# Kernel tuning notes

Measured on AMD Instinct MI355X. Metric: run time of the kernel, lower is better.

## Reference

```python
import math
import jax, jax.numpy as jnp
import numpy as np

N_HEAD = 16
NUM_BUCKETS = 32
MAX_DISTANCE = 2048
NEG_INF = -1e9  # finite stand-in for -inf in masked_fill; rows always have >=1 unmasked entry


def _relative_position_bucket(relative_position, num_buckets=NUM_BUCKETS, max_distance=MAX_DISTANCE):
    # causal (bidirectional=False) T5 bucketing
    rp = -jnp.minimum(relative_position, 0)  # nonneg distances
    max_exact = num_buckets // 2
    is_small = rp < max_exact
    rp_safe = jnp.maximum(rp, 1).astype(jnp.float32)
    large = max_exact + (
        jnp.log(rp_safe / max_exact) / math.log(max_distance / max_exact) * (num_buckets - max_exact)
    ).astype(jnp.int32)
    large = jnp.minimum(large, num_buckets - 1)
    return jnp.where(is_small, rp, large)


def t5_bias(rel_table, T):
    ctx = jnp.arange(T)[:, None]
    mem = jnp.arange(T)[None, :]
    buckets = _relative_position_bucket(mem - ctx)        # [T, T]
    bias = rel_table[buckets]                              # [T, T, H]
    return jnp.transpose(bias, (2, 0, 1))                  # [H, T, T]


def setup_inputs() -> dict:
    key = jax.random.key(0)
    k1, k2, k3, k4 = jax.random.split(key, 4)
    B, T, C = 2, 2048, 1024
    x = jax.random.normal(k1, (B, T, C), dtype=jnp.float32)
    w_qkv = jax.random.normal(k2, (C, 3 * C), dtype=jnp.float32) * (1.0 / math.sqrt(C))
    w_proj = jax.random.normal(k3, (C, C), dtype=jnp.float32) * (1.0 / math.sqrt(C))
    rel_table = jax.random.normal(k4, (NUM_BUCKETS, N_HEAD), dtype=jnp.float32) * 0.02
    return {"x": x, "w_qkv": w_qkv, "w_proj": w_proj, "rel_table": rel_table}


def reference(x, w_qkv, w_proj, rel_table):
    B, T, C = x.shape
    H = N_HEAD
    d = C // H
    qkv = x @ w_qkv                                        # [B, T, 3C]
    q, k, v = jnp.split(qkv, 3, axis=-1)
    q = q.reshape(B, T, H, d).transpose(0, 2, 1, 3)        # [B, H, T, d]
    k = k.reshape(B, T, H, d).transpose(0, 2, 1, 3)
    v = v.reshape(B, T, H, d).transpose(0, 2, 1, 3)

    bias = t5_bias(rel_table, T)                           # [H, T, T]
    causal = jnp.tril(jnp.ones((T, T), dtype=bool))
    bias = jnp.where(causal[None], bias, NEG_INF)          # masked_fill(-inf) on bias

    scores = jnp.einsum("bhqd,bhkd->bhqk", q, k) * (1.0 / math.sqrt(d))
    scores = scores + bias[None]                           # broadcast over batch
    att = jax.nn.softmax(scores, axis=-1)
    y = jnp.einsum("bhqk,bhkd->bhqd", att, v)              # [B, H, T, d]
    y = y.transpose(0, 2, 1, 3).reshape(B, T, C)
    return y @ w_proj
```

## Files before the change

kernel.cpp:

```cpp
#include <hip/hip_runtime.h>
#include <hip/hip_bf16.h>
#include <cstdint>
#include <cstddef>

#define B_  2
#define T_  2048
#define C_  1024
#define H_  16
#define D_  64
#define NEG_INF_ -1e9f

typedef short bf16x8 __attribute__((ext_vector_type(8)));
typedef float f32x4  __attribute__((ext_vector_type(4)));

__device__ __forceinline__ short f2bf(float f) {
  union { float f; unsigned u; } x; x.f = f;
  unsigned r = (x.u + 0x7fffu + ((x.u >> 16) & 1u)) >> 16;
  return (short)r;
}

__device__ __forceinline__ void gload16(const void* g, void* l) {
  __builtin_amdgcn_global_load_lds(
      (const __attribute__((address_space(1))) unsigned int*)g,
      (__attribute__((address_space(3))) unsigned int*)l, 16, 0, 0);
}

__global__ __launch_bounds__(256) void cvt_bf16(const float* __restrict__ in,
                                                short* __restrict__ out, int n4) {
  int i = blockIdx.x * 256 + threadIdx.x;
  if (i < n4) {
    float4 v = ((const float4*)in)[i];
    short4 o;
    o.x = f2bf(v.x); o.y = f2bf(v.y); o.z = f2bf(v.z); o.w = f2bf(v.w);
    ((short4*)out)[i] = o;
  }
}

__global__ __launch_bounds__(256) void transpose_cvt(const float* __restrict__ in,
                                                     short* __restrict__ out,
                                                     int R, int C) {
  __shared__ float tile[32][33];
  int gx = blockIdx.x * 32, gy = blockIdx.y * 32;
  int tx = threadIdx.x, ty = threadIdx.y;
#pragma unroll
  for (int i = 0; i < 4; ++i)
    tile[ty + i * 8][tx] = in[(size_t)(gy + ty + i * 8) * C + gx + tx];
  __syncthreads();
#pragma unroll
  for (int i = 0; i < 4; ++i)
    out[(size_t)(gx + ty + i * 8) * R + gy + tx] = f2bf(tile[tx][ty + i * 8]);
}

__global__ __launch_bounds__(256) void bias_table(const float* __restrict__ rel_table,
                                                  float* __restrict__ btab) {
  int idx = blockIdx.x * 256 + threadIdx.x;
  if (idx >= H_ * T_) return;
  int dist = idx & (T_ - 1);
  int h = idx >> 11;
  int bucket;
  if (dist < 16) {
    bucket = dist;
  } else {
    float rp = (float)dist;
    int large = 16 + (int)(logf(rp * (1.0f / 16.0f)) * (1.0f / logf(128.0f)) * 16.0f);
    bucket = large < 31 ? large : 31;
  }
  btab[idx] = rel_table[bucket * H_ + h];
}

template <int MODE>
__global__ __launch_bounds__(256) void gemm_bt128(
    const short* __restrict__ A, const short* __restrict__ Bt,
    int M, int N, int K,
    short* __restrict__ q_out, short* __restrict__ k_out,
    short* __restrict__ vT_out, float* __restrict__ f_out) {
  __shared__ alignas(16) short As[128 * 64];
  __shared__ alignas(16) short Bs[128 * 64];
  const int tid = threadIdx.x;
  const int w = tid >> 6, lane = tid & 63;
  const int g = lane >> 4, l16 = lane & 15;
  const int wr = w >> 1, wc = w & 1;
  const int m0 = blockIdx.y * 128, n0 = blockIdx.x * 128;

  const char* Ag = (const char*)(A + (size_t)m0 * K);
  const char* Bg = (const char*)(Bt + (size_t)n0 * K);
  char* AsB = (char*)As;
  char* BsB = (char*)Bs;

  int goff[4];
#pragma unroll
  for (int i = 0; i < 4; ++i) {
    int o = i * 256 + tid;
    int row = o >> 3, ch = o & 7;
    goff[i] = row * (K * 2) + ((ch ^ (row & 7)) << 4);
  }

  f32x4 acc[4][4] = {};

  const int nkt = K >> 6;
  for (int kt = 0; kt < nkt; ++kt) {
    __syncthreads();
    const int kbyte = kt << 7;
#pragma unroll
    for (int i = 0; i < 4; ++i)
      gload16(Ag + goff[i] + kbyte, AsB + i * 4096 + w * 1024);
#pragma unroll
    for (int i = 0; i < 4; ++i)
      gload16(Bg + goff[i] + kbyte, BsB + i * 4096 + w * 1024);
    __syncthreads();
#pragma unroll
    for (int kk = 0; kk < 2; ++kk) {
      bf16x8 af[4], bff[4];
#pragma unroll
      for (int m = 0; m < 4; ++m) {
        int r = wr * 64 + m * 16 + l16;
        int off = (r * 128 + kk * 64 + g * 16) ^ ((r & 7) << 4);
        af[m] = *(const bf16x8*)(AsB + off);
      }
#pragma unroll
      for (int n = 0; n < 4; ++n) {
        int c = wc * 64 + n * 16 + l16;
        int off = (c * 128 + kk * 64 + g * 16) ^ ((c & 7) << 4);
        bff[n] = *(const bf16x8*)(BsB + off);
      }
#pragma unroll
      for (int m = 0; m < 4; ++m)
#pragma unroll
        for (int n = 0; n < 4; ++n)
          acc[m][n] = __builtin_amdgcn_mfma_f32_16x16x32_bf16(af[m], bff[n], acc[m][n], 0, 0, 0);
    }
  }

#pragma unroll
  for (int m = 0; m < 4; ++m) {
#pragma unroll
    for (int n = 0; n < 4; ++n) {
      const int colg = n0 + wc * 64 + n * 16 + l16;
#pragma unroll
      for (int r = 0; r < 4; ++r) {
        const int rowg = m0 + wr * 64 + m * 16 + g * 4 + r;
        float v = acc[m][n][r];
        if (MODE == 1) {
          f_out[(size_t)rowg * N + colg] = v;
        } else {
          int part = colg >> 10;
          int within = colg & 1023;
          int h = within >> 6, dd = within & 63;
          int b = rowg >> 11, t = rowg & (T_ - 1);
          size_t bh = (size_t)(b * H_ + h);
          if (part == 0)
            q_out[(bh * T_ + t) * D_ + dd] = f2bf(v * 0.125f);
          else if (part == 1)
            k_out[(bh * T_ + t) * D_ + dd] = f2bf(v);
          else
            vT_out[(bh * D_ + dd) * T_ + t] = f2bf(v);
        }
      }
    }
  }
}

__global__ __launch_bounds__(256) void attn64(
    const short* __restrict__ qb, const short* __restrict__ kb,
    const short* __restrict__ vTb, const float* __restrict__ bias_tab,
    short* __restrict__ yb) {
  __shared__ alignas(16) short Ks[2][64 * 64];
  __shared__ alignas(16) short Vs[2][64 * 64];
  __shared__ alignas(16) short Ps[4][16 * 64];
  __shared__ float biasw[2][2][128];
  const int tid = threadIdx.x;
  const int w = tid >> 6, lane = tid & 63;
  const int g = lane >> 4, l16 = lane & 15;
  const int bh = blockIdx.y;
  const int h = bh & (H_ - 1);
  const int b = bh >> 4;
  const int j = blockIdx.x;
  const int qlo = j, qhi = 31 - j;
  const int q0l = qlo * 64, q0h = qhi * 64;

  const char* kbase = (const char*)(kb + (size_t)bh * T_ * D_);
  const char* vbase = (const char*)(vTb + (size_t)bh * D_ * T_);
  const float* btab = bias_tab + h * T_;

  bf16x8 qfl[2], qfh[2];
  {
    const short* qrl = qb + ((size_t)bh * T_ + q0l + w * 16 + l16) * D_;
    qfl[0] = *(const bf16x8*)(qrl + g * 8);
    qfl[1] = *(const bf16x8*)(qrl + 32 + g * 8);
    const short* qrh = qb + ((size_t)bh * T_ + q0h + w * 16 + l16) * D_;
    qfh[0] = *(const bf16x8*)(qrh + g * 8);
    qfh[1] = *(const bf16x8*)(qrh + 32 + g * 8);
  }

  f32x4 accl[4] = {}, acch[4] = {};
  float ml[4], ll[4], mh[4], lh[4];
#pragma unroll
  for (int r = 0; r < 4; ++r) { ml[r] = mh[r] = -1e30f; ll[r] = lh[r] = 0.f; }

  char* PsB = (char*)&Ps[w][0];

  int krow[2], kch[2];
#pragma unroll
  for (int i = 0; i < 2; ++i) {
    int o = i * 256 + tid;
    krow[i] = o >> 3;
    kch[i] = (o & 7) ^ (krow[i] & 7);
  }

  auto stageKV = [&](int buf, int t) {
    const int kv0 = t * 64;
    char* KsB = (char*)&Ks[buf][0];
    char* VsB = (char*)&Vs[buf][0];
#pragma unroll
    for (int i = 0; i < 2; ++i)
      gload16(kbase + (size_t)(kv0 + krow[i]) * 128 + kch[i] * 16,
              KsB + i * 4096 + w * 1024);
#pragma unroll
    for (int i = 0; i < 2; ++i)
      gload16(vbase + (size_t)krow[i] * (T_ * 2) + kv0 * 2 + kch[i] * 16,
              VsB + i * 4096 + w * 1024);
  };
  auto biasLoad = [&](int t) -> float {
    int i = tid & 127;
    int q0x = (tid >= 128) ? q0h : q0l;
    int d = q0x - t * 64 - 63 + i;
    return (d >= 0 && d < T_) ? btab[d] : NEG_INF_;
  };

  auto computeTile = [&](const char* KsB, const char* VsB, const float* bw,
                         const bf16x8* qf, f32x4* acc, float* mrun, float* lrun) {
    f32x4 s[4];
    __builtin_amdgcn_s_setprio(1);
#pragma unroll
    for (int n = 0; n < 4; ++n) {
      int kvrow = n * 16 + l16;
      int off0 = (kvrow * 128 + g * 16) ^ ((kvrow & 7) << 4);
      int off1 = (kvrow * 128 + 64 + g * 16) ^ ((kvrow & 7) << 4);
      bf16x8 k0 = *(const bf16x8*)(KsB + off0);
      bf16x8 k1 = *(const bf16x8*)(KsB + off1);
      f32x4 z = {};
      z = __builtin_amdgcn_mfma_f32_16x16x32_bf16(qf[0], k0, z, 0, 0, 0);
      z = __builtin_amdgcn_mfma_f32_16x16x32_bf16(qf[1], k1, z, 0, 0, 0);
      s[n] = z;
    }
    __builtin_amdgcn_s_setprio(0);

    float sv[4][4];
    float tmax[4] = {-1e30f, -1e30f, -1e30f, -1e30f};
#pragma unroll
    for (int n = 0; n < 4; ++n) {
#pragma unroll
      for (int r = 0; r < 4; ++r) {
        int idx = 63 + w * 16 + g * 4 + r - n * 16 - l16;
        float val = s[n][r] + bw[idx];
        sv[n][r] = val;
        tmax[r] = fmaxf(tmax[r], val);
      }
    }
#pragma unroll
    for (int r = 0; r < 4; ++r) {
      float v = tmax[r];
      v = fmaxf(v, __shfl_xor(v, 1));
      v = fmaxf(v, __shfl_xor(v, 2));
      v = fmaxf(v, __shfl_xor(v, 4));
      v = fmaxf(v, __shfl_xor(v, 8));
      tmax[r] = v;
    }

    float lt[4];
#pragma unroll
    for (int r = 0; r < 4; ++r) {
      float mnew = fmaxf(mrun[r], tmax[r]);
      float scale = __expf(mrun[r] - mnew);
      mrun[r] = mnew;
      lrun[r] *= scale;
#pragma unroll
      for (int dn = 0; dn < 4; ++dn) acc[dn][r] *= scale;
      float su = 0.f;
#pragma unroll
      for (int n = 0; n < 4; ++n) {
        float p = __expf(sv[n][r] - mnew);
        su += p;
        int row = g * 4 + r, col = n * 16 + l16;
        int off = (row * 128 + col * 2) ^ ((row & 7) << 4);
        *(short*)(PsB + off) = f2bf(p);
      }
      lt[r] = su;
    }
#pragma unroll
    for (int r = 0; r < 4; ++r) {
      float v = lt[r];
      v += __shfl_xor(v, 1);
      v += __shfl_xor(v, 2);
      v += __shfl_xor(v, 4);
      v += __shfl_xor(v, 8);
      lrun[r] += v;
    }

    bf16x8 pf[2];
    {
      int o0 = (l16 * 128 + g * 16) ^ ((l16 & 7) << 4);
      int o1 = (l16 * 128 + 64 + g * 16) ^ ((l16 & 7) << 4);
      pf[0] = *(const bf16x8*)(PsB + o0);
      pf[1] = *(const bf16x8*)(PsB + o1);
    }
    __builtin_amdgcn_s_setprio(1);
#pragma unroll
    for (int dn = 0; dn < 4; ++dn) {
      int drow = dn * 16 + l16;
      int o0 = (drow * 128 + g * 16) ^ ((drow & 7) << 4);
      int o1 = (drow * 128 + 64 + g * 16) ^ ((drow & 7) << 4);
      bf16x8 v0 = *(const bf16x8*)(VsB + o0);
      bf16x8 v1 = *(const bf16x8*)(VsB + o1);
      acc[dn] = __builtin_amdgcn_mfma_f32_16x16x32_bf16(pf[0], v0, acc[dn], 0, 0, 0);
      acc[dn] = __builtin_amdgcn_mfma_f32_16x16x32_bf16(pf[1], v1, acc[dn], 0, 0, 0);
    }
    __builtin_amdgcn_s_setprio(0);
  };

  stageKV(0, 0);
  {
    float bv = biasLoad(0);
    biasw[0][tid >> 7][tid & 127] = bv;
  }
  __syncthreads();

  int cur = 0;
  for (int t = 0; t <= qhi; ++t) {
    const int nxt = cur ^ 1;
    const bool hasnext = (t < qhi);
    float bvn = 0.f;
    if (hasnext) {
      stageKV(nxt, t + 1);
      bvn = biasLoad(t + 1);
    }
    if (t <= qlo)
      computeTile((const char*)&Ks[cur][0], (const char*)&Vs[cur][0],
                  &biasw[cur][0][0], qfl, accl, ml, ll);
    computeTile((const char*)&Ks[cur][0], (const char*)&Vs[cur][0],
                &biasw[cur][1][0], qfh, acch, mh, lh);
    if (hasnext) biasw[nxt][tid >> 7][tid & 127] = bvn;
    __syncthreads();
    cur = nxt;
  }

  auto writeO = [&](int q0x, const f32x4* acc, const float* lrun) {
#pragma unroll
    for (int r = 0; r < 4; ++r) {
      int qg = q0x + w * 16 + g * 4 + r;
      float inv = 1.0f / lrun[r];
      size_t ybase = ((size_t)b * T_ + qg) * C_ + h * D_;
#pragma unroll
      for (int dn = 0; dn < 4; ++dn)
        yb[ybase + dn * 16 + l16] = f2bf(acc[dn][r] * inv);
    }
  };
  writeO(q0l, accl, ll);
  writeO(q0h, acch, lh);
}

extern "C" void kernel_launch(void* const* d_in, const int* in_sizes, int n_in,
                              void* d_out, int out_size, void* d_ws, size_t ws_size,
                              hipStream_t stream) {
  const float* x = (const float*)d_in[0];
  const float* w_qkv = (const float*)d_in[1];
  const float* w_proj = (const float*)d_in[2];
  const float* rel_table = (const float*)d_in[3];
  float* out = (float*)d_out;

  const size_t MB = 1024 * 1024;
  char* ws = (char*)d_ws;
  short* xb     = (short*)(ws);
  short* wqkvT  = (short*)(ws + 8 * MB);
  short* wprojT = (short*)(ws + 14 * MB);
  short* qb     = (short*)(ws + 16 * MB);
  short* kbuf   = (short*)(ws + 24 * MB);
  short* vT     = (short*)(ws + 32 * MB);
  short* yb     = (short*)(ws + 40 * MB);
  float* btab   = (float*)(ws + 48 * MB);

  cvt_bf16<<<4096, 256, 0, stream>>>(x, xb, (B_ * T_ * C_) / 4);
  dim3 tb(32, 8);
  transpose_cvt<<<dim3(96, 32), tb, 0, stream>>>(w_qkv, wqkvT, 1024, 3072);
  transpose_cvt<<<dim3(32, 32), tb, 0, stream>>>(w_proj, wprojT, 1024, 1024);
  bias_table<<<128, 256, 0, stream>>>(rel_table, btab);

  gemm_bt128<0><<<dim3(24, 32), 256, 0, stream>>>(xb, wqkvT, 4096, 3072, 1024,
                                                  qb, kbuf, vT, nullptr);
  attn64<<<dim3(16, 32), 256, 0, stream>>>(qb, kbuf, vT, btab, yb);

  gemm_bt128<1><<<dim3(8, 32), 256, 0, stream>>>(yb, wprojT, 4096, 1024, 1024,
                                                 nullptr, nullptr, nullptr, out);
}
```

Baseline: 220.6 us.

## Interleave lo/hi query tiles, reverse KV order, lazy rescale, defer row-sum reduction

Splits the fused attention tile step into QK^T, softmax and PV phases and interleaves the two query blocks so their independent MFMA chains can overlap, giving each block its own P buffer in shared memory. The KV loop now runs from the diagonal tile backwards, so the running max tends to be set early. A conditional rescale skips the exp/multiply of the accumulators when no row max grows by more than a threshold. The per-tile cross-lane row-sum reduction moves to the final write. This adds LDS and register pressure and a wave-wide vote per tile.

```diff
diff --git a/kernel.cpp b/kernel.cpp
--- a/kernel.cpp
+++ b/kernel.cpp
@@ -166,7 +166,7 @@
     short* __restrict__ yb) {
   __shared__ alignas(16) short Ks[2][64 * 64];
   __shared__ alignas(16) short Vs[2][64 * 64];
-  __shared__ alignas(16) short Ps[4][16 * 64];
+  __shared__ alignas(16) short Ps[4][2][16 * 64];
   __shared__ float biasw[2][2][128];
   const int tid = threadIdx.x;
   const int w = tid >> 6, lane = tid & 63;
@@ -197,7 +197,8 @@
 #pragma unroll
   for (int r = 0; r < 4; ++r) { ml[r] = mh[r] = -1e30f; ll[r] = lh[r] = 0.f; }
 
-  char* PsB = (char*)&Ps[w][0];
+  char* PsLo = (char*)&Ps[w][0][0];
+  char* PsHi = (char*)&Ps[w][1][0];
 
   int krow[2], kch[2];
 #pragma unroll
@@ -227,10 +228,7 @@
     return (d >= 0 && d < T_) ? btab[d] : NEG_INF_;
   };
 
-  auto computeTile = [&](const char* KsB, const char* VsB, const float* bw,
-                         const bf16x8* qf, f32x4* acc, float* mrun, float* lrun) {
-    f32x4 s[4];
-    __builtin_amdgcn_s_setprio(1);
+  auto qkT = [&](const char* KsB, const bf16x8* qf, f32x4* s) {
 #pragma unroll
     for (int n = 0; n < 4; ++n) {
       int kvrow = n * 16 + l16;
@@ -243,8 +241,10 @@
       z = __builtin_amdgcn_mfma_f32_16x16x32_bf16(qf[1], k1, z, 0, 0, 0);
       s[n] = z;
     }
-    __builtin_amdgcn_s_setprio(0);
-
+  };
+
+  auto smT = [&](f32x4* s, const float* bw, char* PsB,
+                 f32x4* acc, float* mrun, float* lrun) {
     float sv[4][4];
     float tmax[4] = {-1e30f, -1e30f, -1e30f, -1e30f};
 #pragma unroll
@@ -266,37 +266,36 @@
       v = fmaxf(v, __shfl_xor(v, 8));
       tmax[r] = v;
     }
-
-    float lt[4];
+    bool nogrow = true;
+#pragma unroll
+    for (int r = 0; r < 4; ++r) nogrow &= (tmax[r] <= mrun[r] + 8.0f);
+    if (!__all(nogrow)) {
+#pragma unroll
+      for (int r = 0; r < 4; ++r) {
+        float mnew = fmaxf(mrun[r], tmax[r]);
+        float scale = __expf(mrun[r] - mnew);
+        mrun[r] = mnew;
+        lrun[r] *= scale;
+#pragma unroll
+        for (int dn = 0; dn < 4; ++dn) acc[dn][r] *= scale;
+      }
+    }
 #pragma unroll
     for (int r = 0; r < 4; ++r) {
-      float mnew = fmaxf(mrun[r], tmax[r]);
-      float scale = __expf(mrun[r] - mnew);
-      mrun[r] = mnew;
-      lrun[r] *= scale;
-#pragma unroll
-      for (int dn = 0; dn < 4; ++dn) acc[dn][r] *= scale;
       float su = 0.f;
 #pragma unroll
       for (int n = 0; n < 4; ++n) {
-        float p = __expf(sv[n][r] - mnew);
+        float p = __expf(sv[n][r] - mrun[r]);
         su += p;
         int row = g * 4 + r, col = n * 16 + l16;
         int off = (row * 128 + col * 2) ^ ((row & 7) << 4);
         *(short*)(PsB + off) = f2bf(p);
       }
-      lt[r] = su;
-    }
-#pragma unroll
-    for (int r = 0; r < 4; ++r) {
-      float v = lt[r];
-      v += __shfl_xor(v, 1);
-      v += __shfl_xor(v, 2);
-      v += __shfl_xor(v, 4);
-      v += __shfl_xor(v, 8);
-      lrun[r] += v;
-    }
-
+      lrun[r] += su;
+    }
+  };
+
+  auto pvT = [&](const char* VsB, const char* PsB, f32x4* acc) {
     bf16x8 pf[2];
     {
       int o0 = (l16 * 128 + g * 16) ^ ((l16 & 7) << 4);
@@ -304,7 +303,6 @@
       pf[0] = *(const bf16x8*)(PsB + o0);
       pf[1] = *(const bf16x8*)(PsB + o1);
     }
-    __builtin_amdgcn_s_setprio(1);
 #pragma unroll
     for (int dn = 0; dn < 4; ++dn) {
       int drow = dn * 16 + l16;
@@ -315,40 +313,63 @@
       acc[dn] = __builtin_amdgcn_mfma_f32_16x16x32_bf16(pf[0], v0, acc[dn], 0, 0, 0);
       acc[dn] = __builtin_amdgcn_mfma_f32_16x16x32_bf16(pf[1], v1, acc[dn], 0, 0, 0);
     }
-    __builtin_amdgcn_s_setprio(0);
-  };
-
-  stageKV(0, 0);
+  };
+
+  stageKV(0, qhi);
   {
-    float bv = biasLoad(0);
+    float bv = biasLoad(qhi);
     biasw[0][tid >> 7][tid & 127] = bv;
   }
   __syncthreads();
 
   int cur = 0;
-  for (int t = 0; t <= qhi; ++t) {
+  for (int t = qhi; t >= 0; --t) {
     const int nxt = cur ^ 1;
-    const bool hasnext = (t < qhi);
+    const bool hasnext = (t > 0);
     float bvn = 0.f;
     if (hasnext) {
-      stageKV(nxt, t + 1);
-      bvn = biasLoad(t + 1);
-    }
-    if (t <= qlo)
-      computeTile((const char*)&Ks[cur][0], (const char*)&Vs[cur][0],
-                  &biasw[cur][0][0], qfl, accl, ml, ll);
-    computeTile((const char*)&Ks[cur][0], (const char*)&Vs[cur][0],
-                &biasw[cur][1][0], qfh, acch, mh, lh);
+      stageKV(nxt, t - 1);
+      bvn = biasLoad(t - 1);
+    }
+    const char* KsB = (const char*)&Ks[cur][0];
+    const char* VsB = (const char*)&Vs[cur][0];
+    if (t <= qlo) {
+      f32x4 sl[4], sh[4];
+      __builtin_amdgcn_s_setprio(1);
+      qkT(KsB, qfl, sl);
+      qkT(KsB, qfh, sh);
+      __builtin_amdgcn_s_setprio(0);
+      smT(sl, &biasw[cur][0][0], PsLo, accl, ml, ll);
+      smT(sh, &biasw[cur][1][0], PsHi, acch, mh, lh);
+      __builtin_amdgcn_s_setprio(1);
+      pvT(VsB, PsLo, accl);
+      pvT(VsB, PsHi, acch);
+      __builtin_amdgcn_s_setprio(0);
+    } else {
+      f32x4 sh[4];
+      __builtin_amdgcn_s_setprio(1);
+      qkT(KsB, qfh, sh);
+      __builtin_amdgcn_s_setprio(0);
+      smT(sh, &biasw[cur][1][0], PsHi, acch, mh, lh);
+      __builtin_amdgcn_s_setprio(1);
+      pvT(VsB, PsHi, acch);
+      __builtin_amdgcn_s_setprio(0);
+    }
     if (hasnext) biasw[nxt][tid >> 7][tid & 127] = bvn;
     __syncthreads();
     cur = nxt;
   }
 
-  auto writeO = [&](int q0x, const f32x4* acc, const float* lrun) {
+  auto writeO = [&](int q0x, const f32x4* acc, float* lrun) {
 #pragma unroll
     for (int r = 0; r < 4; ++r) {
+      float v = lrun[r];
+      v += __shfl_xor(v, 1);
+      v += __shfl_xor(v, 2);
+      v += __shfl_xor(v, 4);
+      v += __shfl_xor(v, 8);
+      float inv = 1.0f / v;
       int qg = q0x + w * 16 + g * 4 + r;
-      float inv = 1.0f / lrun[r];
       size_t ybase = ((size_t)b * T_ + qg) * C_ + h * D_;
 #pragma unroll
       for (int dn = 0; dn < 4; ++dn)
```

After: 256.1 us. 16.1% more time.
